# Kernel tuning notes

Hardware: AMD Instinct MI355X
Metric: run time of the kernel (lower is better)

The kernel has to match this reference:

```python
import jax, jax.numpy as jnp
import numpy as np

B, T, C = 512, 256, 384
HEAD_SIZE = 64
SCALE = np.float32(1.0 / np.sqrt(HEAD_SIZE))


def setup_inputs() -> dict:
    key = jax.random.key(0)
    kx, kq, kk, kv = jax.random.split(key, 4)
    return {
        "x": jax.random.normal(kx, (B, T, C), dtype=jnp.float32),
        "Wq": jax.random.normal(kq, (C, HEAD_SIZE), dtype=jnp.float32) * (C ** -0.5),
        "Wk": jax.random.normal(kk, (C, HEAD_SIZE), dtype=jnp.float32) * (C ** -0.5),
        "Wv": jax.random.normal(kv, (C, HEAD_SIZE), dtype=jnp.float32) * (C ** -0.5),
    }


def reference(x, Wq, Wk, Wv):
    # projections: [B,T,C] @ [C,H] -> [B,T,H]
    q = x @ Wq
    k = x @ Wk
    v = x @ Wv
    # raw scores [B,T,T]
    scores = jnp.einsum("bth,bsh->bts", q, k)
    # causal mask then scale (source masks with -inf before dividing; -inf/8 == -inf)
    causal = jnp.tril(jnp.ones((x.shape[1], x.shape[1]), dtype=bool))
    scores = jnp.where(causal, scores, -jnp.inf) * SCALE
    w = jax.nn.softmax(scores, axis=-1)
    # dropout is identity in eval mode
    return jnp.einsum("bts,bsh->bth", w, v)
```

## Files before the change

kernel.cpp:

```cpp
#include <hip/hip_runtime.h>
#include <hip/hip_bf16.h>
#include <math.h>

#define NB 512
#define NT 256
#define NC 384
#define NH 64

typedef __bf16 bf16x8 __attribute__((ext_vector_type(8)));
typedef unsigned short u16x8 __attribute__((ext_vector_type(8)));
typedef unsigned short u16x4 __attribute__((ext_vector_type(4)));
typedef unsigned int   u32x4 __attribute__((ext_vector_type(4)));
typedef float f32x4 __attribute__((ext_vector_type(4)));

__device__ __forceinline__ unsigned short f2bf(float f) {
    union { float f; unsigned u; } v; v.f = f;
    unsigned r = v.u + 0x7FFFu + ((v.u >> 16) & 1u);
    return (unsigned short)(r >> 16);
}

__device__ __forceinline__ unsigned pack2(float a, float b) {
    return (unsigned)f2bf(a) | ((unsigned)f2bf(b) << 16);
}

__device__ __forceinline__ f32x4 mfma16(bf16x8 a, bf16x8 b, f32x4 c) {
    return __builtin_amdgcn_mfma_f32_16x16x32_bf16(a, b, c, 0, 0, 0);
}

__global__ void prep_w(const float* __restrict__ Wq, const float* __restrict__ Wk,
                       const float* __restrict__ Wv, unsigned short* __restrict__ Wf) {
    const int e = blockIdx.x * 256 + threadIdx.x;
    const int j  = e & 7;
    const int l  = (e >> 3) & 63;
    const int fi = e >> 9;
    const int kk = fi % 12;
    const int n  = fi / 12;
    const int g = l >> 4, col = l & 15;
    const int c = kk * 32 + g * 8 + j;
    const int h = (n & 3) * 16 + col;
    const float* W = (n < 4) ? Wq : (n < 8 ? Wk : Wv);
    Wf[e] = f2bf(W[c * 64 + h]);
}

#define FOFF_Q   0
#define FLDQK    72
#define FOFF_K   18432
#define FOFF_VT  36864
#define FLDVT    264
#define FOFF_XS0 53760
#define FOFF_XS1 66304
#define FLDXS    392
#define FSMEM    78848

__global__ __launch_bounds__(1024, 1) void head_v7(
    const float* __restrict__ x, const unsigned short* __restrict__ Wf,
    float* __restrict__ out)
{
    __shared__ __align__(16) unsigned short SM[FSMEM];

    const int b    = blockIdx.x;
    const int tid  = threadIdx.x;
    const int w    = tid >> 6;
    const int lane = tid & 63;
    const int g    = lane >> 4;
    const int col  = lane & 15;

    const int wq2 = w >> 2;
    const int T = (wq2 == 0) ? w : (wq2 == 1) ? (19 - w) : (wq2 == 2) ? (15 - w) : (w - 4);

    const int pass = w >> 2;
    const int n    = w & 3;
    bf16x8 Bw[12];
    if (w < 12) {
        #pragma unroll
        for (int kk = 0; kk < 12; ++kk)
            Bw[kk] = *reinterpret_cast<const bf16x8*>(
                Wf + ((size_t)((pass * 4 + n) * 12 + kk) * 64 + lane) * 8);
    }

    const int srow[3] = { (tid * 4) / 384, (4096 + tid * 4) / 384, (8192 + tid * 4) / 384 };
    const int scol[3] = { (tid * 4) % 384, (4096 + tid * 4) % 384, (8192 + tid * 4) % 384 };

    {
        const float* xb = x + (size_t)b * NT * NC;
        float4 pre[3];
        #pragma unroll
        for (int k = 0; k < 3; ++k)
            pre[k] = *reinterpret_cast<const float4*>(xb + k * 4096 + tid * 4);
        #pragma unroll
        for (int k = 0; k < 3; ++k) {
            u16x4 u;
            u[0] = f2bf(pre[k].x); u[1] = f2bf(pre[k].y);
            u[2] = f2bf(pre[k].z); u[3] = f2bf(pre[k].w);
            *reinterpret_cast<u16x4*>(&SM[FOFF_XS0 + srow[k] * FLDXS + scol[k]]) = u;
        }
    }
    __syncthreads();

    #pragma unroll 1
    for (int ch = 0; ch < 8; ++ch) {
        float4 nxt[3];
        if (ch < 7) {
            const float* xb = x + ((size_t)b * NT + (ch + 1) * 32) * NC;
            #pragma unroll
            for (int k = 0; k < 3; ++k)
                nxt[k] = *reinterpret_cast<const float4*>(xb + k * 4096 + tid * 4);
        }

        const int xsbase = (ch & 1) ? FOFF_XS1 : FOFF_XS0;
        if (w < 12) {
            #pragma unroll
            for (int rt = 0; rt < 2; ++rt) {
                const int tile = ch * 2 + rt;
                f32x4 acc = (f32x4){0.f, 0.f, 0.f, 0.f};
                #pragma unroll
                for (int kk = 0; kk < 12; ++kk) {
                    const bf16x8 xf = *reinterpret_cast<const bf16x8*>(
                        &SM[xsbase + (rt * 16 + col) * FLDXS + kk * 32 + g * 8]);
                    acc = mfma16(xf, Bw[kk], acc);
                }
                const int tb = tile * 16 + g * 4;
                if (pass < 2) {
                    const int base = (pass == 0) ? FOFF_Q : FOFF_K;
                    #pragma unroll
                    for (int r = 0; r < 4; ++r)
                        SM[base + (tb + r) * FLDQK + n * 16 + col] = f2bf(acc[r]);
                } else {
                    #pragma unroll
                    for (int r = 0; r < 4; ++r)
                        SM[FOFF_VT + (n * 16 + col) * FLDVT + tb + r] = f2bf(acc[r]);
                }
            }
        }
        __syncthreads();

        if (ch < 7) {
            const int nb = ((ch + 1) & 1) ? FOFF_XS1 : FOFF_XS0;
            #pragma unroll
            for (int k = 0; k < 3; ++k) {
                u16x4 u;
                u[0] = f2bf(nxt[k].x); u[1] = f2bf(nxt[k].y);
                u[2] = f2bf(nxt[k].z); u[3] = f2bf(nxt[k].w);
                *reinterpret_cast<u16x4*>(&SM[nb + srow[k] * FLDXS + scol[k]]) = u;
            }
        }
        __syncthreads();
    }

    const int hi_half = (lane >> 5) & 1;
    const int srcA = ((lane >> 4) & 1) * 32 + col;
    const int srcB = srcA + 16;

    bf16x8 qb[2];
    #pragma unroll
    for (int kk = 0; kk < 2; ++kk)
        qb[kk] = *reinterpret_cast<const bf16x8*>(
            &SM[FOFF_Q + (T * 16 + col) * FLDQK + kk * 32 + g * 8]);

    f32x4 sc[16];
    #pragma unroll
    for (int nt = 0; nt < 16; ++nt) {
        if (nt <= T) {
            f32x4 a = {0.f, 0.f, 0.f, 0.f};
            const bf16x8 ka0 = *reinterpret_cast<const bf16x8*>(
                &SM[FOFF_K + (nt * 16 + col) * FLDQK + g * 8]);
            const bf16x8 ka1 = *reinterpret_cast<const bf16x8*>(
                &SM[FOFF_K + (nt * 16 + col) * FLDQK + 32 + g * 8]);
            a = mfma16(ka0, qb[0], a);
            a = mfma16(ka1, qb[1], a);
            sc[nt] = a;
        }
    }

    float m = -INFINITY;
    #pragma unroll
    for (int nt = 0; nt < 16; ++nt) {
        if (nt <= T) {
            #pragma unroll
            for (int r = 0; r < 4; ++r) {
                float v = sc[nt][r] * 0.125f;
                if (nt == T && (4 * g + r) > col) v = -INFINITY;
                sc[nt][r] = v;
                m = fmaxf(m, v);
            }
        }
    }
    m = fmaxf(m, __shfl_xor(m, 16));
    m = fmaxf(m, __shfl_xor(m, 32));
    float s = 0.f;
    #pragma unroll
    for (int nt = 0; nt < 16; ++nt) {
        if (nt <= T) {
            #pragma unroll
            for (int r = 0; r < 4; ++r) {
                const float p = __expf(sc[nt][r] - m);
                sc[nt][r] = p;
                s += p;
            }
        }
    }
    s += __shfl_xor(s, 16);
    s += __shfl_xor(s, 32);
    const float inv = 1.0f / s;

    unsigned P4lo[16], P4hi[16];
    #pragma unroll
    for (int nt = 0; nt < 16; ++nt) {
        if (nt <= T) {
            P4lo[nt] = pack2(sc[nt][0] * inv, sc[nt][1] * inv);
            P4hi[nt] = pack2(sc[nt][2] * inv, sc[nt][3] * inv);
        } else { P4lo[nt] = 0u; P4hi[nt] = 0u; }
    }

    f32x4 oacc[4];
    #pragma unroll
    for (int nn = 0; nn < 4; ++nn) oacc[nn] = (f32x4){0.f, 0.f, 0.f, 0.f};
    #pragma unroll
    for (int cpv = 0; cpv < 8; ++cpv) {
        if (cpv <= (T >> 1)) {
            const unsigned a0 = __shfl(P4lo[2 * cpv],     srcA, 64);
            const unsigned a1 = __shfl(P4lo[2 * cpv + 1], srcA, 64);
            const unsigned b0 = __shfl(P4hi[2 * cpv],     srcA, 64);
            const unsigned b1 = __shfl(P4hi[2 * cpv + 1], srcA, 64);
            const unsigned c0 = __shfl(P4lo[2 * cpv],     srcB, 64);
            const unsigned c1 = __shfl(P4lo[2 * cpv + 1], srcB, 64);
            const unsigned d0 = __shfl(P4hi[2 * cpv],     srcB, 64);
            const unsigned d1 = __shfl(P4hi[2 * cpv + 1], srcB, 64);
            u32x4 wv;
            wv[0] = hi_half ? a1 : a0;
            wv[1] = hi_half ? b1 : b0;
            wv[2] = hi_half ? c1 : c0;
            wv[3] = hi_half ? d1 : d0;
            const bf16x8 pa = __builtin_bit_cast(bf16x8, wv);
            #pragma unroll
            for (int nn = 0; nn < 4; ++nn) {
                const bf16x8 vb = *reinterpret_cast<const bf16x8*>(
                    &SM[FOFF_VT + (nn * 16 + col) * FLDVT + cpv * 32 + g * 8]);
                oacc[nn] = mfma16(pa, vb, oacc[nn]);
            }
        }
    }

    #pragma unroll
    for (int nn = 0; nn < 4; ++nn)
        #pragma unroll
        for (int r = 0; r < 4; ++r)
            out[((size_t)b * NT + T * 16 + 4 * g + r) * NH + nn * 16 + col] = oacc[nn][r];
}

extern "C" void kernel_launch(void* const* d_in, const int* in_sizes, int n_in,
                              void* d_out, int out_size, void* d_ws, size_t ws_size,
                              hipStream_t stream) {
    (void)in_sizes; (void)n_in; (void)out_size; (void)ws_size;
    const float* x  = (const float*)d_in[0];
    const float* wq = (const float*)d_in[1];
    const float* wk = (const float*)d_in[2];
    const float* wv = (const float*)d_in[3];
    float* o = (float*)d_out;

    unsigned short* Wf = (unsigned short*)d_ws;
    prep_w <<<dim3(288), dim3(256),  0, stream>>>(wq, wk, wv, Wf);
    head_v7<<<dim3(NB),  dim3(1024), 0, stream>>>(x, Wf, o);
}
```

Before: 58.17 us.

## Process two batches per block and prefetch next batch during attention

Each workgroup now handles two consecutive batch elements, with grid size halved to 256 blocks. The weight fragments are loaded into registers once per block and reused for both batches. The first x chunk of the second batch is prefetched from global memory while the first batch's attention phase runs. This targets per-block setup cost and the exposed load latency between phases. The trade-off is that only 256 blocks are launched on a 256-CU device, which removes tail-balancing slack and serializes the two batches within a CU.

```diff
diff --git a/kernel.cpp b/kernel.cpp
--- a/kernel.cpp
+++ b/kernel.cpp
@@ -52,13 +52,12 @@
 #define FLDXS    392
 #define FSMEM    78848
 
-__global__ __launch_bounds__(1024, 1) void head_v7(
+__global__ __launch_bounds__(1024, 1) void head_v8(
     const float* __restrict__ x, const unsigned short* __restrict__ Wf,
     float* __restrict__ out)
 {
     __shared__ __align__(16) unsigned short SM[FSMEM];
 
-    const int b    = blockIdx.x;
     const int tid  = threadIdx.x;
     const int w    = tid >> 6;
     const int lane = tid & 63;
@@ -82,7 +81,7 @@
     const int scol[3] = { (tid * 4) % 384, (4096 + tid * 4) % 384, (8192 + tid * 4) % 384 };
 
     {
-        const float* xb = x + (size_t)b * NT * NC;
+        const float* xb = x + (size_t)(blockIdx.x * 2) * NT * NC;
         float4 pre[3];
         #pragma unroll
         for (int k = 0; k < 3; ++k)
@@ -98,154 +97,179 @@
     __syncthreads();
 
     #pragma unroll 1
-    for (int ch = 0; ch < 8; ++ch) {
-        float4 nxt[3];
-        if (ch < 7) {
-            const float* xb = x + ((size_t)b * NT + (ch + 1) * 32) * NC;
+    for (int bi = 0; bi < 2; ++bi) {
+        const int b = blockIdx.x * 2 + bi;
+        const float* xb = x + (size_t)b * NT * NC;
+
+        #pragma unroll 1
+        for (int ch = 0; ch < 8; ++ch) {
+            float4 nxt[3];
+            if (ch < 7) {
+                const float* xc = xb + (size_t)(ch + 1) * 32 * NC;
+                #pragma unroll
+                for (int k = 0; k < 3; ++k)
+                    nxt[k] = *reinterpret_cast<const float4*>(xc + k * 4096 + tid * 4);
+            }
+
+            const int xsbase = (ch & 1) ? FOFF_XS1 : FOFF_XS0;
+            if (w < 12) {
+                #pragma unroll
+                for (int rt = 0; rt < 2; ++rt) {
+                    const int tile = ch * 2 + rt;
+                    f32x4 acc = (f32x4){0.f, 0.f, 0.f, 0.f};
+                    #pragma unroll
+                    for (int kk = 0; kk < 12; ++kk) {
+                        const bf16x8 xf = *reinterpret_cast<const bf16x8*>(
+                            &SM[xsbase + (rt * 16 + col) * FLDXS + kk * 32 + g * 8]);
+                        acc = mfma16(xf, Bw[kk], acc);
+                    }
+                    const int tb = tile * 16 + g * 4;
+                    if (pass < 2) {
+                        const int base = (pass == 0) ? FOFF_Q : FOFF_K;
+                        #pragma unroll
+                        for (int r = 0; r < 4; ++r)
+                            SM[base + (tb + r) * FLDQK + n * 16 + col] = f2bf(acc[r]);
+                    } else {
+                        #pragma unroll
+                        for (int r = 0; r < 4; ++r)
+                            SM[FOFF_VT + (n * 16 + col) * FLDVT + tb + r] = f2bf(acc[r]);
+                    }
+                }
+            }
+            __syncthreads();
+
+            if (ch < 7) {
+                const int nb = ((ch + 1) & 1) ? FOFF_XS1 : FOFF_XS0;
+                #pragma unroll
+                for (int k = 0; k < 3; ++k) {
+                    u16x4 u;
+                    u[0] = f2bf(nxt[k].x); u[1] = f2bf(nxt[k].y);
+                    u[2] = f2bf(nxt[k].z); u[3] = f2bf(nxt[k].w);
+                    *reinterpret_cast<u16x4*>(&SM[nb + srow[k] * FLDXS + scol[k]]) = u;
+                }
+            }
+            __syncthreads();
+        }
+
+        float4 nb0[3];
+        if (bi == 0) {
+            const float* xn = x + (size_t)(b + 1) * NT * NC;
             #pragma unroll
             for (int k = 0; k < 3; ++k)
-                nxt[k] = *reinterpret_cast<const float4*>(xb + k * 4096 + tid * 4);
-        }
-
-        const int xsbase = (ch & 1) ? FOFF_XS1 : FOFF_XS0;
-        if (w < 12) {
+                nb0[k] = *reinterpret_cast<const float4*>(xn + k * 4096 + tid * 4);
+        }
+
+        const int hi_half = (lane >> 5) & 1;
+        const int srcA = ((lane >> 4) & 1) * 32 + col;
+        const int srcB = srcA + 16;
+
+        bf16x8 qb[2];
+        #pragma unroll
+        for (int kk = 0; kk < 2; ++kk)
+            qb[kk] = *reinterpret_cast<const bf16x8*>(
+                &SM[FOFF_Q + (T * 16 + col) * FLDQK + kk * 32 + g * 8]);
+
+        f32x4 sc[16];
+        #pragma unroll
+        for (int nt = 0; nt < 16; ++nt) {
+            if (nt <= T) {
+                f32x4 a = {0.f, 0.f, 0.f, 0.f};
+                const bf16x8 ka0 = *reinterpret_cast<const bf16x8*>(
+                    &SM[FOFF_K + (nt * 16 + col) * FLDQK + g * 8]);
+                const bf16x8 ka1 = *reinterpret_cast<const bf16x8*>(
+                    &SM[FOFF_K + (nt * 16 + col) * FLDQK + 32 + g * 8]);
+                a = mfma16(ka0, qb[0], a);
+                a = mfma16(ka1, qb[1], a);
+                sc[nt] = a;
+            }
+        }
+
+        float m = -INFINITY;
+        #pragma unroll
+        for (int nt = 0; nt < 16; ++nt) {
+            if (nt <= T) {
+                #pragma unroll
+                for (int r = 0; r < 4; ++r) {
+                    float v = sc[nt][r] * 0.125f;
+                    if (nt == T && (4 * g + r) > col) v = -INFINITY;
+                    sc[nt][r] = v;
+                    m = fmaxf(m, v);
+                }
+            }
+        }
+        m = fmaxf(m, __shfl_xor(m, 16));
+        m = fmaxf(m, __shfl_xor(m, 32));
+        float s = 0.f;
+        #pragma unroll
+        for (int nt = 0; nt < 16; ++nt) {
+            if (nt <= T) {
+                #pragma unroll
+                for (int r = 0; r < 4; ++r) {
+                    const float p = __expf(sc[nt][r] - m);
+                    sc[nt][r] = p;
+                    s += p;
+                }
+            }
+        }
+        s += __shfl_xor(s, 16);
+        s += __shfl_xor(s, 32);
+        const float inv = 1.0f / s;
+
+        unsigned P4lo[16], P4hi[16];
+        #pragma unroll
+        for (int nt = 0; nt < 16; ++nt) {
+            if (nt <= T) {
+                P4lo[nt] = pack2(sc[nt][0] * inv, sc[nt][1] * inv);
+                P4hi[nt] = pack2(sc[nt][2] * inv, sc[nt][3] * inv);
+            } else { P4lo[nt] = 0u; P4hi[nt] = 0u; }
+        }
+
+        f32x4 oacc[4];
+        #pragma unroll
+        for (int nn = 0; nn < 4; ++nn) oacc[nn] = (f32x4){0.f, 0.f, 0.f, 0.f};
+        #pragma unroll
+        for (int cpv = 0; cpv < 8; ++cpv) {
+            if (cpv <= (T >> 1)) {
+                const unsigned a0 = __shfl(P4lo[2 * cpv],     srcA, 64);
+                const unsigned a1 = __shfl(P4lo[2 * cpv + 1], srcA, 64);
+                const unsigned b0 = __shfl(P4hi[2 * cpv],     srcA, 64);
+                const unsigned b1 = __shfl(P4hi[2 * cpv + 1], srcA, 64);
+                const unsigned c0 = __shfl(P4lo[2 * cpv],     srcB, 64);
+                const unsigned c1 = __shfl(P4lo[2 * cpv + 1], srcB, 64);
+                const unsigned d0 = __shfl(P4hi[2 * cpv],     srcB, 64);
+                const unsigned d1 = __shfl(P4hi[2 * cpv + 1], srcB, 64);
+                u32x4 wv;
+                wv[0] = hi_half ? a1 : a0;
+                wv[1] = hi_half ? b1 : b0;
+                wv[2] = hi_half ? c1 : c0;
+                wv[3] = hi_half ? d1 : d0;
+                const bf16x8 pa = __builtin_bit_cast(bf16x8, wv);
+                #pragma unroll
+                for (int nn = 0; nn < 4; ++nn) {
+                    const bf16x8 vb = *reinterpret_cast<const bf16x8*>(
+                        &SM[FOFF_VT + (nn * 16 + col) * FLDVT + cpv * 32 + g * 8]);
+                    oacc[nn] = mfma16(pa, vb, oacc[nn]);
+                }
+            }
+        }
+
+        #pragma unroll
+        for (int nn = 0; nn < 4; ++nn)
             #pragma unroll
-            for (int rt = 0; rt < 2; ++rt) {
-                const int tile = ch * 2 + rt;
-                f32x4 acc = (f32x4){0.f, 0.f, 0.f, 0.f};
-                #pragma unroll
-                for (int kk = 0; kk < 12; ++kk) {
-                    const bf16x8 xf = *reinterpret_cast<const bf16x8*>(
-                        &SM[xsbase + (rt * 16 + col) * FLDXS + kk * 32 + g * 8]);
-                    acc = mfma16(xf, Bw[kk], acc);
-                }
-                const int tb = tile * 16 + g * 4;
-                if (pass < 2) {
-                    const int base = (pass == 0) ? FOFF_Q : FOFF_K;
-                    #pragma unroll
-                    for (int r = 0; r < 4; ++r)
-                        SM[base + (tb + r) * FLDQK + n * 16 + col] = f2bf(acc[r]);
-                } else {
-                    #pragma unroll
-                    for (int r = 0; r < 4; ++r)
-                        SM[FOFF_VT + (n * 16 + col) * FLDVT + tb + r] = f2bf(acc[r]);
-                }
-            }
-        }
-        __syncthreads();
-
-        if (ch < 7) {
-            const int nb = ((ch + 1) & 1) ? FOFF_XS1 : FOFF_XS0;
+            for (int r = 0; r < 4; ++r)
+                out[((size_t)b * NT + T * 16 + 4 * g + r) * NH + nn * 16 + col] = oacc[nn][r];
+
+        if (bi == 0) {
             #pragma unroll
             for (int k = 0; k < 3; ++k) {
                 u16x4 u;
-                u[0] = f2bf(nxt[k].x); u[1] = f2bf(nxt[k].y);
-                u[2] = f2bf(nxt[k].z); u[3] = f2bf(nxt[k].w);
-                *reinterpret_cast<u16x4*>(&SM[nb + srow[k] * FLDXS + scol[k]]) = u;
-            }
-        }
-        __syncthreads();
+                u[0] = f2bf(nb0[k].x); u[1] = f2bf(nb0[k].y);
+                u[2] = f2bf(nb0[k].z); u[3] = f2bf(nb0[k].w);
+                *reinterpret_cast<u16x4*>(&SM[FOFF_XS0 + srow[k] * FLDXS + scol[k]]) = u;
+            }
+            __syncthreads();
+        }
     }
-
-    const int hi_half = (lane >> 5) & 1;
-    const int srcA = ((lane >> 4) & 1) * 32 + col;
-    const int srcB = srcA + 16;
-
-    bf16x8 qb[2];
-    #pragma unroll
-    for (int kk = 0; kk < 2; ++kk)
-        qb[kk] = *reinterpret_cast<const bf16x8*>(
-            &SM[FOFF_Q + (T * 16 + col) * FLDQK + kk * 32 + g * 8]);
-
-    f32x4 sc[16];
-    #pragma unroll
-    for (int nt = 0; nt < 16; ++nt) {
-        if (nt <= T) {
-            f32x4 a = {0.f, 0.f, 0.f, 0.f};
-            const bf16x8 ka0 = *reinterpret_cast<const bf16x8*>(
-                &SM[FOFF_K + (nt * 16 + col) * FLDQK + g * 8]);
-            const bf16x8 ka1 = *reinterpret_cast<const bf16x8*>(
-                &SM[FOFF_K + (nt * 16 + col) * FLDQK + 32 + g * 8]);
-            a = mfma16(ka0, qb[0], a);
-            a = mfma16(ka1, qb[1], a);
-            sc[nt] = a;
-        }
-    }
-
-    float m = -INFINITY;
-    #pragma unroll
-    for (int nt = 0; nt < 16; ++nt) {
-        if (nt <= T) {
-            #pragma unroll
-            for (int r = 0; r < 4; ++r) {
-                float v = sc[nt][r] * 0.125f;
-                if (nt == T && (4 * g + r) > col) v = -INFINITY;
-                sc[nt][r] = v;
-                m = fmaxf(m, v);
-            }
-        }
-    }
-    m = fmaxf(m, __shfl_xor(m, 16));
-    m = fmaxf(m, __shfl_xor(m, 32));
-    float s = 0.f;
-    #pragma unroll
-    for (int nt = 0; nt < 16; ++nt) {
-        if (nt <= T) {
-            #pragma unroll
-            for (int r = 0; r < 4; ++r) {
-                const float p = __expf(sc[nt][r] - m);
-                sc[nt][r] = p;
-                s += p;
-            }
-        }
-    }
-    s += __shfl_xor(s, 16);
-    s += __shfl_xor(s, 32);
-    const float inv = 1.0f / s;
-
-    unsigned P4lo[16], P4hi[16];
-    #pragma unroll
-    for (int nt = 0; nt < 16; ++nt) {
-        if (nt <= T) {
-            P4lo[nt] = pack2(sc[nt][0] * inv, sc[nt][1] * inv);
-            P4hi[nt] = pack2(sc[nt][2] * inv, sc[nt][3] * inv);
-        } else { P4lo[nt] = 0u; P4hi[nt] = 0u; }
-    }
-
-    f32x4 oacc[4];
-    #pragma unroll
-    for (int nn = 0; nn < 4; ++nn) oacc[nn] = (f32x4){0.f, 0.f, 0.f, 0.f};
-    #pragma unroll
-    for (int cpv = 0; cpv < 8; ++cpv) {
-        if (cpv <= (T >> 1)) {
-            const unsigned a0 = __shfl(P4lo[2 * cpv],     srcA, 64);
-            const unsigned a1 = __shfl(P4lo[2 * cpv + 1], srcA, 64);
-            const unsigned b0 = __shfl(P4hi[2 * cpv],     srcA, 64);
-            const unsigned b1 = __shfl(P4hi[2 * cpv + 1], srcA, 64);
-            const unsigned c0 = __shfl(P4lo[2 * cpv],     srcB, 64);
-            const unsigned c1 = __shfl(P4lo[2 * cpv + 1], srcB, 64);
-            const unsigned d0 = __shfl(P4hi[2 * cpv],     srcB, 64);
-            const unsigned d1 = __shfl(P4hi[2 * cpv + 1], srcB, 64);
-            u32x4 wv;
-            wv[0] = hi_half ? a1 : a0;
-            wv[1] = hi_half ? b1 : b0;
-            wv[2] = hi_half ? c1 : c0;
-            wv[3] = hi_half ? d1 : d0;
-            const bf16x8 pa = __builtin_bit_cast(bf16x8, wv);
-            #pragma unroll
-            for (int nn = 0; nn < 4; ++nn) {
-                const bf16x8 vb = *reinterpret_cast<const bf16x8*>(
-                    &SM[FOFF_VT + (nn * 16 + col) * FLDVT + cpv * 32 + g * 8]);
-                oacc[nn] = mfma16(pa, vb, oacc[nn]);
-            }
-        }
-    }
-
-    #pragma unroll
-    for (int nn = 0; nn < 4; ++nn)
-        #pragma unroll
-        for (int r = 0; r < 4; ++r)
-            out[((size_t)b * NT + T * 16 + 4 * g + r) * NH + nn * 16 + col] = oacc[nn][r];
 }
 
 extern "C" void kernel_launch(void* const* d_in, const int* in_sizes, int n_in,
@@ -259,6 +283,6 @@
     float* o = (float*)d_out;
 
     unsigned short* Wf = (unsigned short*)d_ws;
-    prep_w <<<dim3(288), dim3(256),  0, stream>>>(wq, wk, wv, Wf);
-    head_v7<<<dim3(NB),  dim3(1024), 0, stream>>>(x, Wf, o);
-}
+    prep_w <<<dim3(288),    dim3(256),  0, stream>>>(wq, wk, wv, Wf);
+    head_v8<<<dim3(NB / 2), dim3(1024), 0, stream>>>(x, Wf, o);
+}
```

After: 192.5 us. +230.9%, slower.
